# Optimization experiments

Hardware: AMD Instinct MI355X
Metric: run time of the kernel (lower is better)

Reference implementation:

```python
import jax, jax.numpy as jnp
import numpy as np

N_NODES = 40000
N_EDGES = 640000
D = 128
N_GRAPHS = 64


def gcn_conv(x, W, b, edge_index):
    """PyG-style GCNConv: add self-loops, symmetric norm, linear, scatter-add."""
    n = x.shape[0]
    loops = jnp.arange(n, dtype=edge_index.dtype)
    src = jnp.concatenate([edge_index[0], loops])  # message sources (x_j)
    dst = jnp.concatenate([edge_index[1], loops])  # aggregation targets
    # deg computed over targets (col) with unit edge weights, incl. self-loops
    deg = jax.ops.segment_sum(jnp.ones_like(src, dtype=x.dtype), dst, num_segments=n)
    dinv = jnp.where(deg > 0, jax.lax.rsqrt(jnp.maximum(deg, 1.0)), 0.0)
    norm = dinv[src] * dinv[dst]  # [E+N]
    h = x @ W  # [N, d_out]
    out = jax.ops.segment_sum(norm[:, None] * h[src], dst, num_segments=n)
    return out + b


def global_mean_pool(x, batch, num_graphs):
    summed = jax.ops.segment_sum(x, batch, num_segments=num_graphs)
    counts = jax.ops.segment_sum(jnp.ones((x.shape[0],), x.dtype), batch, num_segments=num_graphs)
    return summed / jnp.maximum(counts, 1.0)[:, None]


def setup_inputs() -> dict:
    key = jax.random.key(0)
    ks = jax.random.split(key, 6)
    x = jax.random.normal(ks[0], (N_NODES, D), dtype=jnp.float32)
    edge_index = jax.random.randint(ks[1], (2, N_EDGES), 0, N_NODES)
    batch = jnp.sort(jax.random.randint(ks[2], (N_NODES,), 0, N_GRAPHS))
    s = 1.0 / np.sqrt(D)
    W1 = jax.random.normal(ks[3], (D, D), dtype=jnp.float32) * s
    W2 = jax.random.normal(ks[4], (D, D), dtype=jnp.float32) * s
    b1 = jnp.zeros((D,), jnp.float32)
    b2 = jnp.zeros((D,), jnp.float32)
    return {"x": x, "edge_index": edge_index, "batch": batch,
            "W1": W1, "b1": b1, "W2": W2, "b2": b2}


def reference(x, edge_index, batch, W1, b1, W2, b2):
    h = jax.nn.relu(gcn_conv(x, W1, b1, edge_index))
    h = gcn_conv(h, W2, b2, edge_index)  # no ReLU on last layer
    return global_mean_pool(h, batch, N_GRAPHS)
```

## Files before the change

kernel.cpp:

```cpp
#include <hip/hip_runtime.h>

#define D 128
#define N_GRAPHS 64

typedef unsigned int uint32;
typedef __attribute__((ext_vector_type(8))) _Float16 f16x8;
typedef __attribute__((ext_vector_type(4))) float f32x4;

__device__ __forceinline__ float hl(uint32 u) {
    return (float)__builtin_bit_cast(_Float16, (unsigned short)(u & 0xFFFF));
}
__device__ __forceinline__ float hh(uint32 u) {
    return (float)__builtin_bit_cast(_Float16, (unsigned short)(u >> 16));
}
__device__ __forceinline__ uint32 h2pair(float a, float b) {
    unsigned short ua = __builtin_bit_cast(unsigned short, (_Float16)a);
    unsigned short ub = __builtin_bit_cast(unsigned short, (_Float16)b);
    return (uint32)ua | ((uint32)ub << 16);
}

__global__ __launch_bounds__(256) void prep_kernel(int* __restrict__ cnt,
                                                   const float* __restrict__ W1,
                                                   uint32* __restrict__ Wh, int n) {
    int i = blockIdx.x * 256 + threadIdx.x;
    if (i < n) {
        cnt[i] = 0;
    } else if (i < n + D * (D / 2)) {
        int j = i - n;
        int nn = j & 127, kd = j >> 7;
        float v0 = W1[(size_t)(2 * kd) * D + nn];
        float v1 = W1[(size_t)(2 * kd + 1) * D + nn];
        Wh[nn * 64 + kd] = h2pair(v0, v1);
    }
}


#define GBM 64

__global__ __launch_bounds__(256) void count_gemm_kernel(
    const float* __restrict__ A, const uint32* __restrict__ Wh,
    uint32* __restrict__ hb, int M, int gemmBlocks,
    const int* __restrict__ dst, int* __restrict__ cnt,
    int* __restrict__ rank, int E) {
    __shared__ uint32 lds[64 * 68];

    if (blockIdx.x >= gemmBlocks) {
        int e = (blockIdx.x - gemmBlocks) * 256 + threadIdx.x;
        if (e < E) rank[e] = atomicAdd(&cnt[dst[e]], 1);
        return;
    }

    uint32* As = lds;
    int tid = threadIdx.x;
    int row0 = blockIdx.x * GBM;

#pragma unroll
    for (int j = 0; j < 8; ++j) {
        int idx = tid + j * 256;
        int r = idx >> 5, c4 = idx & 31;
        float4 v = make_float4(0.f, 0.f, 0.f, 0.f);
        if (row0 + r < M) v = *(const float4*)&A[(size_t)(row0 + r) * D + c4 * 4];
        As[r * 68 + c4 * 2 + 0] = h2pair(v.x, v.y);
        As[r * 68 + c4 * 2 + 1] = h2pair(v.z, v.w);
    }
    __syncthreads();

    int wave = tid >> 6, lane = tid & 63;
    int quad = lane >> 4, l16 = lane & 15;
    int wr = (wave & 1) * 32;
    int wc = (wave >> 1) * 64;
    f32x4 acc[2][4];
#pragma unroll
    for (int mi = 0; mi < 2; ++mi)
#pragma unroll
        for (int ni = 0; ni < 4; ++ni) acc[mi][ni] = (f32x4){0.f, 0.f, 0.f, 0.f};

#pragma unroll
    for (int ks = 0; ks < 4; ++ks) {
        int kd = ks * 16 + quad * 4;
        f16x8 a0 = *(f16x8*)&As[(wr + l16) * 68 + kd];
        f16x8 a1 = *(f16x8*)&As[(wr + 16 + l16) * 68 + kd];
        f16x8 b0 = *(const f16x8*)&Wh[(wc + l16) * 64 + kd];
        f16x8 b1 = *(const f16x8*)&Wh[(wc + 16 + l16) * 64 + kd];
        f16x8 b2 = *(const f16x8*)&Wh[(wc + 32 + l16) * 64 + kd];
        f16x8 b3 = *(const f16x8*)&Wh[(wc + 48 + l16) * 64 + kd];
        acc[0][0] = __builtin_amdgcn_mfma_f32_16x16x32_f16(a0, b0, acc[0][0], 0, 0, 0);
        acc[0][1] = __builtin_amdgcn_mfma_f32_16x16x32_f16(a0, b1, acc[0][1], 0, 0, 0);
        acc[0][2] = __builtin_amdgcn_mfma_f32_16x16x32_f16(a0, b2, acc[0][2], 0, 0, 0);
        acc[0][3] = __builtin_amdgcn_mfma_f32_16x16x32_f16(a0, b3, acc[0][3], 0, 0, 0);
        acc[1][0] = __builtin_amdgcn_mfma_f32_16x16x32_f16(a1, b0, acc[1][0], 0, 0, 0);
        acc[1][1] = __builtin_amdgcn_mfma_f32_16x16x32_f16(a1, b1, acc[1][1], 0, 0, 0);
        acc[1][2] = __builtin_amdgcn_mfma_f32_16x16x32_f16(a1, b2, acc[1][2], 0, 0, 0);
        acc[1][3] = __builtin_amdgcn_mfma_f32_16x16x32_f16(a1, b3, acc[1][3], 0, 0, 0);
    }
    __syncthreads();

    unsigned short* cs = (unsigned short*)lds;
#pragma unroll
    for (int mi = 0; mi < 2; ++mi)
#pragma unroll
        for (int ni = 0; ni < 4; ++ni)
#pragma unroll
            for (int r = 0; r < 4; ++r) {
                int row = wr + mi * 16 + quad * 4 + r;
                int col2 = wc + ni * 16 + l16;
                cs[row * 128 + col2] =
                    __builtin_bit_cast(unsigned short, (_Float16)acc[mi][ni][r]);
            }
    __syncthreads();
#pragma unroll
    for (int j = 0; j < 4; ++j) {
        int idx = tid + j * 256;
        int r = idx >> 4, q = idx & 15;
        if (row0 + r < M)
            *(uint4*)&hb[(size_t)(row0 + r) * 64 + q * 4] = *(uint4*)&lds[r * 64 + q * 4];
    }
}


__global__ __launch_bounds__(1024) void scanA_kernel(const int* __restrict__ cnt,
                                                     int* __restrict__ rowptr,
                                                     int* __restrict__ tot,
                                                     float* __restrict__ dinv, int n) {
    __shared__ int swave[16];
    int t = threadIdx.x;
    int lane = t & 63, wave = t >> 6;
    int i = blockIdx.x * 1024 + t;
    int orig = (i < n) ? cnt[i] : 0;
    int v = orig;
#pragma unroll
    for (int off = 1; off < 64; off <<= 1) {
        int u = __shfl_up(v, off, 64);
        if (lane >= off) v += u;
    }
    if (lane == 63) swave[wave] = v;
    __syncthreads();
    if (wave == 0) {
        int wv = (lane < 16) ? swave[lane] : 0;
#pragma unroll
        for (int off = 1; off < 16; off <<= 1) {
            int u = __shfl_up(wv, off, 64);
            if (lane >= off) wv += u;
        }
        if (lane < 16) swave[lane] = wv;
    }
    if (i < n) dinv[i] = rsqrtf((float)(orig + 1));
    __syncthreads();
    int incl = v + ((wave > 0) ? swave[wave - 1] : 0);
    if (i < n) rowptr[i] = incl - orig;
    if (t == 1023) tot[blockIdx.x] = incl;
}

__global__ __launch_bounds__(1024) void scanB_kernel(int* __restrict__ rowptr,
                                                     const int* __restrict__ tot,
                                                     int n, int nchunks) {
    __shared__ int soff;
    int b = blockIdx.x, t = threadIdx.x;
    if (t == 0) {
        int o = 0;
        for (int j = 0; j < b; ++j) o += tot[j];
        soff = o;
    }
    __syncthreads();
    int i = b * 1024 + t;
    if (i < n) rowptr[i] += soff;
    if (b == 0 && t == 0) {
        int o = 0;
        for (int j = 0; j < nchunks; ++j) o += tot[j];
        rowptr[n] = o;
    }
}

__global__ void fill_kernel(const int* __restrict__ src, const int* __restrict__ dst,
                            const int* __restrict__ rowptr, const int* __restrict__ rank,
                            int* __restrict__ col, int E) {
    int e = blockIdx.x * blockDim.x + threadIdx.x;
    if (e < E) col[rowptr[dst[e]] + rank[e]] = src[e];
}


__global__ __launch_bounds__(128) void agg_kernel(const uint32* __restrict__ hb,
                                                  const int* __restrict__ rowptr,
                                                  const int* __restrict__ col,
                                                  const float* __restrict__ dinv,
                                                  const float* __restrict__ bias,
                                                  uint32* __restrict__ h1, int n) {
    int tid = threadIdx.x;
    int lane32 = tid & 31;
    int slot = tid >> 5;
    int node = blockIdx.x * 4 + slot;
    if (node >= n) return;
    const uint2* __restrict__ h2 = (const uint2*)hb;

    float di = dinv[node];
    float ws = di * di;
    uint2 su = h2[(size_t)node * 32 + lane32];
    float a0 = ws * hl(su.x), a1 = ws * hh(su.x);
    float a2 = ws * hl(su.y), a3 = ws * hh(su.y);

    int k = rowptr[node], end = rowptr[node + 1];
    for (; k + 8 <= end; k += 8) {
        uint2 v[8];
        float w[8];
#pragma unroll
        for (int j = 0; j < 8; ++j) {
            int s = col[k + j];
            w[j] = dinv[s] * di;
            v[j] = h2[(size_t)s * 32 + lane32];
        }
#pragma unroll
        for (int j = 0; j < 8; ++j) {
            a0 = fmaf(w[j], hl(v[j].x), a0);
            a1 = fmaf(w[j], hh(v[j].x), a1);
            a2 = fmaf(w[j], hl(v[j].y), a2);
            a3 = fmaf(w[j], hh(v[j].y), a3);
        }
    }
    for (; k < end; ++k) {
        int s = col[k];
        float w = dinv[s] * di;
        uint2 v = h2[(size_t)s * 32 + lane32];
        a0 = fmaf(w, hl(v.x), a0);
        a1 = fmaf(w, hh(v.x), a1);
        a2 = fmaf(w, hl(v.y), a2);
        a3 = fmaf(w, hh(v.y), a3);
    }

    float4 b4 = ((const float4*)bias)[lane32];
    a0 = fmaxf(a0 + b4.x, 0.f);
    a1 = fmaxf(a1 + b4.y, 0.f);
    a2 = fmaxf(a2 + b4.z, 0.f);
    a3 = fmaxf(a3 + b4.w, 0.f);
    uint2 o;
    o.x = h2pair(a0, a1);
    o.y = h2pair(a2, a3);
    ((uint2*)h1)[(size_t)node * 32 + lane32] = o;
}

#define P2K 32

__global__ __launch_bounds__(256) void agg2pool_kernel(const uint32* __restrict__ h1,
                                                       const int* __restrict__ rowptr,
                                                       const int* __restrict__ col,
                                                       const float* __restrict__ dinv,
                                                       const int* __restrict__ batch,
                                                       float* __restrict__ Ppart, int n) {
    __shared__ float pool[8][D];
    __shared__ int srange[2];
    int t = threadIdx.x;
    int g = blockIdx.x >> 5;
    int kslice = blockIdx.x & 31;
    int lane32 = t & 31, slot = t >> 5;

    if (t == 0) {
        int lo = 0, hi = n;
        while (lo < hi) { int mid = (lo + hi) >> 1; if (batch[mid] < g) lo = mid + 1; else hi = mid; }
        srange[0] = lo;
        int g1 = g + 1;
        lo = 0; hi = n;
        while (lo < hi) { int mid = (lo + hi) >> 1; if (batch[mid] < g1) lo = mid + 1; else hi = mid; }
        srange[1] = lo;
    }
    *(float4*)&pool[slot][lane32 * 4] = make_float4(0.f, 0.f, 0.f, 0.f);
    __syncthreads();

    int lb = srange[0], cntg = srange[1] - srange[0];
    int a = lb + (int)(((long long)cntg * kslice) >> 5);
    int b = lb + (int)(((long long)cntg * (kslice + 1)) >> 5);
    const uint2* __restrict__ h2 = (const uint2*)h1;

    for (int node = a + slot; node < b; node += 8) {
        float di = dinv[node];
        float ws = di * di;
        uint2 su = h2[(size_t)node * 32 + lane32];
        float a0 = ws * hl(su.x), a1 = ws * hh(su.x);
        float a2 = ws * hl(su.y), a3 = ws * hh(su.y);

        int k = rowptr[node], end = rowptr[node + 1];
        for (; k + 8 <= end; k += 8) {
            uint2 v[8];
            float w[8];
#pragma unroll
            for (int j = 0; j < 8; ++j) {
                int s = col[k + j];
                w[j] = dinv[s] * di;
                v[j] = h2[(size_t)s * 32 + lane32];
            }
#pragma unroll
            for (int j = 0; j < 8; ++j) {
                a0 = fmaf(w[j], hl(v[j].x), a0);
                a1 = fmaf(w[j], hh(v[j].x), a1);
                a2 = fmaf(w[j], hl(v[j].y), a2);
                a3 = fmaf(w[j], hh(v[j].y), a3);
            }
        }
        for (; k < end; ++k) {
            int s = col[k];
            float w = dinv[s] * di;
            uint2 v = h2[(size_t)s * 32 + lane32];
            a0 = fmaf(w, hl(v.x), a0);
            a1 = fmaf(w, hh(v.x), a1);
            a2 = fmaf(w, hl(v.y), a2);
            a3 = fmaf(w, hh(v.y), a3);
        }
        float4 p = *(float4*)&pool[slot][lane32 * 4];
        p.x += a0; p.y += a1; p.z += a2; p.w += a3;
        *(float4*)&pool[slot][lane32 * 4] = p;
    }
    __syncthreads();
    if (t < D) {
        float s = 0.f;
#pragma unroll
        for (int sl = 0; sl < 8; ++sl) s += pool[sl][t];
        Ppart[(size_t)blockIdx.x * D + t] = s;
    }
}

__global__ __launch_bounds__(256) void out_kernel(const float* __restrict__ Ppart,
                                                  const float* __restrict__ W2,
                                                  const float* __restrict__ b2,
                                                  const int* __restrict__ batch, int n,
                                                  float* __restrict__ out) {
    __shared__ float gs[D];
    __shared__ float part[2][D];
    __shared__ float srinv;
    int g = blockIdx.x, t = threadIdx.x;
    int f = t & 127, half = t >> 7;
    if (t == 0) {
        int lo = 0, hi = n;
        while (lo < hi) { int mid = (lo + hi) >> 1; if (batch[mid] < g) lo = mid + 1; else hi = mid; }
        int lb = lo;
        int g1 = g + 1;
        lo = 0; hi = n;
        while (lo < hi) { int mid = (lo + hi) >> 1; if (batch[mid] < g1) lo = mid + 1; else hi = mid; }
        int cg = lo - lb;
        srinv = (cg > 0) ? 1.0f / (float)cg : 0.0f;
    }
    float s = 0.f;
    int j0 = half * (P2K / 2);
#pragma unroll
    for (int j = j0; j < j0 + P2K / 2; ++j)
        s += Ppart[((size_t)g * P2K + j) * D + f];
    part[half][f] = s;
    __syncthreads();
    if (half == 0) gs[f] = part[0][f] + part[1][f];
    __syncthreads();
    float acc = 0.f;
    int k0 = half * (D / 2);
#pragma unroll 8
    for (int k = k0; k < k0 + D / 2; ++k) acc = fmaf(gs[k], W2[k * D + f], acc);
    part[half][f] = acc;
    __syncthreads();
    if (half == 0) {
        float a = part[0][f] + part[1][f];
        float r = srinv;
        out[g * D + f] = (r > 0.f) ? fmaf(a, r, b2[f]) : 0.f;
    }
}


extern "C" void kernel_launch(void* const* d_in, const int* in_sizes, int n_in,
                              void* d_out, int out_size, void* d_ws, size_t ws_size,
                              hipStream_t stream) {
    const float* x  = (const float*)d_in[0];
    const int*   ei = (const int*)d_in[1];
    const int*   batch = (const int*)d_in[2];
    const float* W1 = (const float*)d_in[3];
    const float* b1 = (const float*)d_in[4];
    const float* W2 = (const float*)d_in[5];
    const float* b2 = (const float*)d_in[6];
    float* out = (float*)d_out;

    const int n = in_sizes[2];
    const int E = in_sizes[1] / 2;
    const int* src = ei;
    const int* dst = ei + E;

    char* ws = (char*)d_ws;
    size_t off = 0;
    auto carve = [&](size_t bytes) {
        size_t o = off;
        off = (off + bytes + 255) & ~(size_t)255;
        return (void*)(ws + o);
    };
    int*    cnt    = (int*)carve((size_t)n * 4);
    int*    rowptr = (int*)carve((size_t)(n + 1) * 4);
    float*  dinv   = (float*)carve((size_t)n * 4);
    int*    col    = (int*)carve((size_t)E * 4);
    uint32* hb     = (uint32*)carve((size_t)n * D * 2);
    uint32* h1     = (uint32*)carve((size_t)n * D * 2);
    int*    tot    = (int*)carve(64 * 4);
    int*    rank   = (int*)carve((size_t)E * 4);
    uint32* Wh     = (uint32*)carve((size_t)D * (D / 2) * 4);
    float*  Ppart  = (float*)hb;
    (void)ws_size;

    const int nchunks = (n + 1023) >> 10;

    prep_kernel<<<(n + D * (D / 2) + 255) / 256, 256, 0, stream>>>(cnt, W1, Wh, n);

    const int gemmBlocks = (n + GBM - 1) / GBM;
    const int countBlocks = (E + 255) / 256;
    count_gemm_kernel<<<gemmBlocks + countBlocks, 256, 0, stream>>>(
        x, Wh, hb, n, gemmBlocks, dst, cnt, rank, E);

    scanA_kernel<<<nchunks, 1024, 0, stream>>>(cnt, rowptr, tot, dinv, n);
    scanB_kernel<<<nchunks, 1024, 0, stream>>>(rowptr, tot, n, nchunks);
    fill_kernel<<<(E + 255) / 256, 256, 0, stream>>>(src, dst, rowptr, rank, col, E);

    agg_kernel<<<(n + 3) / 4, 128, 0, stream>>>(hb, rowptr, col, dinv, b1, h1, n);

    agg2pool_kernel<<<N_GRAPHS * P2K, 256, 0, stream>>>(h1, rowptr, col, dinv, batch,
                                                        Ppart, n);
    out_kernel<<<N_GRAPHS, 256, 0, stream>>>(Ppart, W2, b2, batch, n, out);
}
```

Baseline: 201.2 us.

## Split fused second aggregation and pooling into per-node agg and separate pool kernels

```diff
diff --git a/kernel.cpp b/kernel.cpp
--- a/kernel.cpp
+++ b/kernel.cpp
@@ -237,21 +237,65 @@
     ((uint2*)h1)[(size_t)node * 32 + lane32] = o;
 }
 
-#define P2K 32
-
-__global__ __launch_bounds__(256) void agg2pool_kernel(const uint32* __restrict__ h1,
-                                                       const int* __restrict__ rowptr,
-                                                       const int* __restrict__ col,
-                                                       const float* __restrict__ dinv,
-                                                       const int* __restrict__ batch,
-                                                       float* __restrict__ Ppart, int n) {
-    __shared__ float pool[8][D];
+
+__global__ __launch_bounds__(128) void agg2_kernel(const uint32* __restrict__ h1,
+                                                   const int* __restrict__ rowptr,
+                                                   const int* __restrict__ col,
+                                                   const float* __restrict__ dinv,
+                                                   float* __restrict__ P2, int n) {
+    int tid = threadIdx.x;
+    int lane32 = tid & 31;
+    int slot = tid >> 5;
+    int node = blockIdx.x * 4 + slot;
+    if (node >= n) return;
+    const uint2* __restrict__ h2 = (const uint2*)h1;
+
+    float di = dinv[node];
+    float ws = di * di;
+    uint2 su = h2[(size_t)node * 32 + lane32];
+    float a0 = ws * hl(su.x), a1 = ws * hh(su.x);
+    float a2 = ws * hl(su.y), a3 = ws * hh(su.y);
+
+    int k = rowptr[node], end = rowptr[node + 1];
+    for (; k + 8 <= end; k += 8) {
+        uint2 v[8];
+        float w[8];
+#pragma unroll
+        for (int j = 0; j < 8; ++j) {
+            int s = col[k + j];
+            w[j] = dinv[s] * di;
+            v[j] = h2[(size_t)s * 32 + lane32];
+        }
+#pragma unroll
+        for (int j = 0; j < 8; ++j) {
+            a0 = fmaf(w[j], hl(v[j].x), a0);
+            a1 = fmaf(w[j], hh(v[j].x), a1);
+            a2 = fmaf(w[j], hl(v[j].y), a2);
+            a3 = fmaf(w[j], hh(v[j].y), a3);
+        }
+    }
+    for (; k < end; ++k) {
+        int s = col[k];
+        float w = dinv[s] * di;
+        uint2 v = h2[(size_t)s * 32 + lane32];
+        a0 = fmaf(w, hl(v.x), a0);
+        a1 = fmaf(w, hh(v.x), a1);
+        a2 = fmaf(w, hl(v.y), a2);
+        a3 = fmaf(w, hh(v.y), a3);
+    }
+
+    *(float4*)&P2[(size_t)node * D + lane32 * 4] = make_float4(a0, a1, a2, a3);
+}
+
+#define PSL 16
+
+__global__ __launch_bounds__(128) void pool_kernel(const float* __restrict__ P2,
+                                                   const int* __restrict__ batch,
+                                                   float* __restrict__ Ppart, int n) {
     __shared__ int srange[2];
     int t = threadIdx.x;
-    int g = blockIdx.x >> 5;
-    int kslice = blockIdx.x & 31;
-    int lane32 = t & 31, slot = t >> 5;
-
+    int g = blockIdx.x >> 4;
+    int kslice = blockIdx.x & 15;
     if (t == 0) {
         int lo = 0, hi = n;
         while (lo < hi) { int mid = (lo + hi) >> 1; if (batch[mid] < g) lo = mid + 1; else hi = mid; }
@@ -261,59 +305,22 @@
         while (lo < hi) { int mid = (lo + hi) >> 1; if (batch[mid] < g1) lo = mid + 1; else hi = mid; }
         srange[1] = lo;
     }
-    *(float4*)&pool[slot][lane32 * 4] = make_float4(0.f, 0.f, 0.f, 0.f);
-    __syncthreads();
-
+    __syncthreads();
     int lb = srange[0], cntg = srange[1] - srange[0];
-    int a = lb + (int)(((long long)cntg * kslice) >> 5);
-    int b = lb + (int)(((long long)cntg * (kslice + 1)) >> 5);
-    const uint2* __restrict__ h2 = (const uint2*)h1;
-
-    for (int node = a + slot; node < b; node += 8) {
-        float di = dinv[node];
-        float ws = di * di;
-        uint2 su = h2[(size_t)node * 32 + lane32];
-        float a0 = ws * hl(su.x), a1 = ws * hh(su.x);
-        float a2 = ws * hl(su.y), a3 = ws * hh(su.y);
-
-        int k = rowptr[node], end = rowptr[node + 1];
-        for (; k + 8 <= end; k += 8) {
-            uint2 v[8];
-            float w[8];
-#pragma unroll
-            for (int j = 0; j < 8; ++j) {
-                int s = col[k + j];
-                w[j] = dinv[s] * di;
-                v[j] = h2[(size_t)s * 32 + lane32];
-            }
-#pragma unroll
-            for (int j = 0; j < 8; ++j) {
-                a0 = fmaf(w[j], hl(v[j].x), a0);
-                a1 = fmaf(w[j], hh(v[j].x), a1);
-                a2 = fmaf(w[j], hl(v[j].y), a2);
-                a3 = fmaf(w[j], hh(v[j].y), a3);
-            }
-        }
-        for (; k < end; ++k) {
-            int s = col[k];
-            float w = dinv[s] * di;
-            uint2 v = h2[(size_t)s * 32 + lane32];
-            a0 = fmaf(w, hl(v.x), a0);
-            a1 = fmaf(w, hh(v.x), a1);
-            a2 = fmaf(w, hl(v.y), a2);
-            a3 = fmaf(w, hh(v.y), a3);
-        }
-        float4 p = *(float4*)&pool[slot][lane32 * 4];
-        p.x += a0; p.y += a1; p.z += a2; p.w += a3;
-        *(float4*)&pool[slot][lane32 * 4] = p;
-    }
-    __syncthreads();
-    if (t < D) {
-        float s = 0.f;
-#pragma unroll
-        for (int sl = 0; sl < 8; ++sl) s += pool[sl][t];
-        Ppart[(size_t)blockIdx.x * D + t] = s;
-    }
+    int a = lb + (int)(((long long)cntg * kslice) >> 4);
+    int b = lb + (int)(((long long)cntg * (kslice + 1)) >> 4);
+
+    float s = 0.f;
+    int node = a;
+    for (; node + 4 <= b; node += 4) {
+        float v0 = P2[(size_t)(node + 0) * D + t];
+        float v1 = P2[(size_t)(node + 1) * D + t];
+        float v2 = P2[(size_t)(node + 2) * D + t];
+        float v3 = P2[(size_t)(node + 3) * D + t];
+        s += (v0 + v1) + (v2 + v3);
+    }
+    for (; node < b; ++node) s += P2[(size_t)node * D + t];
+    Ppart[(size_t)blockIdx.x * D + t] = s;
 }
 
 __global__ __launch_bounds__(256) void out_kernel(const float* __restrict__ Ppart,
@@ -337,10 +344,10 @@
         srinv = (cg > 0) ? 1.0f / (float)cg : 0.0f;
     }
     float s = 0.f;
-    int j0 = half * (P2K / 2);
-#pragma unroll
-    for (int j = j0; j < j0 + P2K / 2; ++j)
-        s += Ppart[((size_t)g * P2K + j) * D + f];
+    int j0 = half * (PSL / 2);
+#pragma unroll
+    for (int j = j0; j < j0 + PSL / 2; ++j)
+        s += Ppart[((size_t)g * PSL + j) * D + f];
     part[half][f] = s;
     __syncthreads();
     if (half == 0) gs[f] = part[0][f] + part[1][f];
@@ -392,6 +399,7 @@
     int*    tot    = (int*)carve(64 * 4);
     int*    rank   = (int*)carve((size_t)E * 4);
     uint32* Wh     = (uint32*)carve((size_t)D * (D / 2) * 4);
+    float*  P2     = (float*)carve((size_t)n * D * 4);
     float*  Ppart  = (float*)hb;
     (void)ws_size;
 
@@ -410,7 +418,7 @@
 
     agg_kernel<<<(n + 3) / 4, 128, 0, stream>>>(hb, rowptr, col, dinv, b1, h1, n);
 
-    agg2pool_kernel<<<N_GRAPHS * P2K, 256, 0, stream>>>(h1, rowptr, col, dinv, batch,
-                                                        Ppart, n);
+    agg2_kernel<<<(n + 3) / 4, 128, 0, stream>>>(h1, rowptr, col, dinv, P2, n);
+    pool_kernel<<<N_GRAPHS * PSL, 128, 0, stream>>>(P2, batch, Ppart, n);
     out_kernel<<<N_GRAPHS, 256, 0, stream>>>(Ppart, W2, b2, batch, n, out);
 }
```

Result: faster. 193.1 us (-4.0%).
